# Performance work log

Hardware: AMD Instinct MI355X
Metric: run time of the kernel (lower is better)

The kernel has to match this reference:

```python
import jax, jax.numpy as jnp
import numpy as np

NEG_SLOPE = 0.1  # LeakyReLU alpha from __init__
EPS = 1e-5


def setup_inputs() -> dict:
    key = jax.random.key(0)
    k1, k2, k3, k4, k5 = jax.random.split(key, 5)
    N, E, DIN, DOUT = 10000, 160000, 1024, 1024
    x = jax.random.normal(k1, (N, DIN), dtype=jnp.float32)
    W = jax.random.normal(k2, (DIN, DOUT), dtype=jnp.float32) * 0.02  # xavier-ish gain
    a = jax.random.normal(k3, (1, 2 * DOUT), dtype=jnp.float32) * 0.02
    src = jax.random.randint(k4, (E,), 0, N, dtype=jnp.int64)  # edge rows i
    dst = jax.random.randint(k5, (E,), 0, N, dtype=jnp.int64)  # edge cols j
    return {"x": x, "W": W, "a": a, "src": src, "dst": dst}


def reference(x, W, a, src, dst):
    N = x.shape[0]
    d = W.shape[1]
    h = x @ W                                   # [N, d]
    # a @ cat(h_src, h_dst)^T == (h @ a_l)[src] + (h @ a_r)[dst]
    a_l, a_r = a[0, :d], a[0, d:]
    al = h @ a_l                                # [N]
    ar = h @ a_r                                # [N]
    e = jnp.exp(-jax.nn.leaky_relu(al[src] + ar[dst], negative_slope=NEG_SLOPE))  # [E]
    # sparse rowsum: A @ ones  ->  segment_sum of e over rows
    rowsum = jax.ops.segment_sum(e, src, num_segments=N)          # [N]
    # sparse aggregate: A @ h  (dropout = identity in eval mode)
    h_prime = jax.ops.segment_sum(e[:, None] * h[dst], src, num_segments=N)  # [N, d]
    h_prime = h_prime / (rowsum[:, None] + EPS)
    return jax.nn.elu(h_prime)  # concat=True branch
```

## Files before the change

### kernel.cpp

```cpp
#include <hip/hip_runtime.h>
#include <hip/hip_bf16.h>
#include <stdint.h>
#include <math.h>

#define DK 1024
#define DN 1024
#define CAP 64

typedef __attribute__((ext_vector_type(8))) short bf16x8;
typedef __attribute__((ext_vector_type(4))) float f32x4;

__device__ __forceinline__ unsigned short f2bf(float f) {
  union { float f; uint32_t u; } v; v.f = f;
  uint32_t r = v.u + 0x7FFFu + ((v.u >> 16) & 1u);
  return (unsigned short)(r >> 16);
}
__device__ __forceinline__ float bf2f(unsigned short b) {
  union { uint32_t u; float f; } v; v.u = ((uint32_t)b) << 16; return v.f;
}

__device__ __forceinline__ void gload_lds16(const void* g, void* l) {
  __builtin_amdgcn_global_load_lds((const __attribute__((address_space(1))) unsigned int*)g,
                                   (__attribute__((address_space(3))) unsigned int*)l,
                                   16, 0, 0);
}

__device__ __forceinline__ void block_reduce2(float& pl, float& pr) {
#pragma unroll
  for (int off = 32; off >= 1; off >>= 1) {
    pl += __shfl_down(pl, off);
    pr += __shfl_down(pr, off);
  }
  __shared__ float sl[4], sr[4];
  int w = threadIdx.x >> 6, lane = threadIdx.x & 63;
  if (lane == 0) { sl[w] = pl; sr[w] = pr; }
  __syncthreads();
  if (threadIdx.x == 0) {
    pl = sl[0] + sl[1] + sl[2] + sl[3];
    pr = sr[0] + sr[1] + sr[2] + sr[3];
  }
}

__global__ __launch_bounds__(256) void wvec_kernel(const float* __restrict__ W,
                                                   const float* __restrict__ a,
                                                   float* __restrict__ wl,
                                                   float* __restrict__ wr,
                                                   int* __restrict__ cnt, int M) {
  int idx = blockIdx.x * 256 + threadIdx.x;
  if (idx < M) cnt[idx] = 0;
  int k = blockIdx.x;
  int tid = threadIdx.x;
  float4 wv = ((const float4*)(W + (size_t)k * DN))[tid];
  float4 l4 = ((const float4*)a)[tid];
  float4 r4 = ((const float4*)(a + DN))[tid];
  float pl = wv.x * l4.x + wv.y * l4.y + wv.z * l4.z + wv.w * l4.w;
  float pr = wv.x * r4.x + wv.y * r4.y + wv.z * r4.z + wv.w * r4.w;
  block_reduce2(pl, pr);
  if (tid == 0) { wl[k] = pl; wr[k] = pr; }
}

__global__ __launch_bounds__(256) void prep_kernel(const float* __restrict__ x,
                                                   unsigned short* __restrict__ xb,
                                                   const float* __restrict__ W,
                                                   unsigned short* __restrict__ Wt,
                                                   const float* __restrict__ wl,
                                                   const float* __restrict__ wr,
                                                   float* __restrict__ al,
                                                   float* __restrict__ ar,
                                                   int M) {
  if ((int)blockIdx.x < M) {
    int row = blockIdx.x;
    int tid = threadIdx.x;
    float4 v = ((const float4*)(x + (size_t)row * DK))[tid];
    ushort4 o;
    o.x = f2bf(v.x); o.y = f2bf(v.y); o.z = f2bf(v.z); o.w = f2bf(v.w);
    ((ushort4*)(xb + (size_t)row * DK))[tid] = o;
    float4 l4 = ((const float4*)wl)[tid];
    float4 r4 = ((const float4*)wr)[tid];
    float pl = v.x * l4.x + v.y * l4.y + v.z * l4.z + v.w * l4.w;
    float pr = v.x * r4.x + v.y * r4.y + v.z * r4.z + v.w * r4.w;
    block_reduce2(pl, pr);
    if (tid == 0) { al[row] = pl; ar[row] = pr; }
  } else {
    __shared__ float t[32][33];
    int bid = blockIdx.x - M;
    int tx = threadIdx.x & 31, ty = threadIdx.x >> 5;
    int bk = (bid & 31) * 32, bn = (bid >> 5) * 32;
#pragma unroll
    for (int rr = 0; rr < 4; ++rr) {
      int row = ty + rr * 8;
      t[row][tx] = W[(size_t)(bk + row) * DN + bn + tx];
    }
    __syncthreads();
#pragma unroll
    for (int rr = 0; rr < 4; ++rr) {
      int row = ty + rr * 8;
      Wt[(size_t)(bn + row) * DK + bk + tx] = f2bf(t[tx][row]);
    }
  }
}

__global__ __launch_bounds__(256) void gemm_kernel(const unsigned short* __restrict__ A,
                                                   const unsigned short* __restrict__ Bt,
                                                   unsigned short* __restrict__ Hb,
                                                   int M) {
  __shared__ unsigned short As[128 * 32];
  __shared__ unsigned short Bs[128 * 32];
  const int tid = threadIdx.x;
  const int w = tid >> 6, lane = tid & 63;
  const int r = lane & 15, q = lane >> 4;
  const int m0 = blockIdx.x * 128, n0 = blockIdx.y * 128;
  const int wr = (w >> 1) * 64, wc = (w & 1) * 64;

  const int c0 = w * 64 + lane;
  const int rowA0 = c0 >> 2, g0 = c0 & 3;
  const int rowA1 = rowA0 + 64;
  int gr0 = m0 + rowA0; if (gr0 >= M) gr0 = M - 1;
  int gr1 = m0 + rowA1; if (gr1 >= M) gr1 = M - 1;
  const unsigned short* gA0 = A + (size_t)gr0 * DK + g0 * 8;
  const unsigned short* gA1 = A + (size_t)gr1 * DK + g0 * 8;
  const unsigned short* gB0 = Bt + (size_t)(n0 + rowA0) * DK + g0 * 8;
  const unsigned short* gB1 = Bt + (size_t)(n0 + rowA1) * DK + g0 * 8;
  unsigned short* lA0 = As + w * 512;
  unsigned short* lA1 = As + 2048 + w * 512;
  unsigned short* lB0 = Bs + w * 512;
  unsigned short* lB1 = Bs + 2048 + w * 512;

  const f32x4 zero = {0.f, 0.f, 0.f, 0.f};
  f32x4 acc[4][4];
#pragma unroll
  for (int i = 0; i < 4; ++i)
#pragma unroll
    for (int j = 0; j < 4; ++j) acc[i][j] = zero;

  for (int k0 = 0; k0 < DK; k0 += 32) {
    gload_lds16(gA0, lA0);
    gload_lds16(gA1, lA1);
    gload_lds16(gB0, lB0);
    gload_lds16(gB1, lB1);
    gA0 += 32; gA1 += 32; gB0 += 32; gB1 += 32;
    __syncthreads();

    bf16x8 af[4], bfr[4];
#pragma unroll
    for (int i = 0; i < 4; ++i)
      af[i] = *(const bf16x8*)&As[(wr + i * 16 + r) * 32 + q * 8];
#pragma unroll
    for (int j = 0; j < 4; ++j)
      bfr[j] = *(const bf16x8*)&Bs[(wc + j * 16 + r) * 32 + q * 8];
#pragma unroll
    for (int i = 0; i < 4; ++i)
#pragma unroll
      for (int j = 0; j < 4; ++j)
        acc[i][j] = __builtin_amdgcn_mfma_f32_16x16x32_bf16(af[i], bfr[j], acc[i][j], 0, 0, 0);
    __syncthreads();
  }

#pragma unroll
  for (int i = 0; i < 4; ++i) {
#pragma unroll
    for (int reg = 0; reg < 4; ++reg) {
      int m = m0 + wr + i * 16 + q * 4 + reg;
      if (m < M) {
#pragma unroll
        for (int j = 0; j < 4; ++j) {
          int n = n0 + wc + j * 16 + r;
          Hb[(size_t)m * DN + n] = f2bf(acc[i][j][reg]);
        }
      }
    }
  }
}

__global__ __launch_bounds__(256) void edge_kernel(const int* __restrict__ src,
                                                   const int* __restrict__ dst,
                                                   const float* __restrict__ al,
                                                   const float* __restrict__ ar,
                                                   int* __restrict__ cnt,
                                                   int* __restrict__ bdst,
                                                   float* __restrict__ be, int E) {
  int i = blockIdx.x * 256 + threadIdx.x;
  if (i < E) {
    int s = src[i], d = dst[i];
    float v = al[s] + ar[d];
    float lr = v > 0.f ? v : 0.1f * v;
    float e = expf(-lr);
    int pos = atomicAdd(&cnt[s], 1);
    if (pos < CAP) {
      bdst[(s << 6) + pos] = d;
      be[(s << 6) + pos] = e;
    }
  }
}

__global__ __launch_bounds__(256) void aggregate_kernel(const int* __restrict__ cnt,
                                                        const int* __restrict__ bdst,
                                                        const float* __restrict__ be,
                                                        const unsigned short* __restrict__ Hb,
                                                        float* __restrict__ out, int M) {
  int row = blockIdx.x;
  int tid = threadIdx.x;
  int n = cnt[row]; if (n > CAP) n = CAP;
  int base = row << 6;
  size_t coff = (size_t)tid * 4;
  float a0 = 0.f, a1 = 0.f, a2 = 0.f, a3 = 0.f, rs = 0.f;
  int p = 0;
  for (; p + 8 <= n; p += 8) {
    int4 da = *(const int4*)(bdst + base + p);
    int4 db = *(const int4*)(bdst + base + p + 4);
    float4 ea = *(const float4*)(be + base + p);
    float4 eb = *(const float4*)(be + base + p + 4);
    ushort4 h0 = *(const ushort4*)&Hb[(size_t)da.x * DN + coff];
    ushort4 h1 = *(const ushort4*)&Hb[(size_t)da.y * DN + coff];
    ushort4 h2 = *(const ushort4*)&Hb[(size_t)da.z * DN + coff];
    ushort4 h3 = *(const ushort4*)&Hb[(size_t)da.w * DN + coff];
    ushort4 h4 = *(const ushort4*)&Hb[(size_t)db.x * DN + coff];
    ushort4 h5 = *(const ushort4*)&Hb[(size_t)db.y * DN + coff];
    ushort4 h6 = *(const ushort4*)&Hb[(size_t)db.z * DN + coff];
    ushort4 h7 = *(const ushort4*)&Hb[(size_t)db.w * DN + coff];
    rs += ((ea.x + ea.y) + (ea.z + ea.w)) + ((eb.x + eb.y) + (eb.z + eb.w));
    a0 += ea.x * bf2f(h0.x) + ea.y * bf2f(h1.x) + ea.z * bf2f(h2.x) + ea.w * bf2f(h3.x)
        + eb.x * bf2f(h4.x) + eb.y * bf2f(h5.x) + eb.z * bf2f(h6.x) + eb.w * bf2f(h7.x);
    a1 += ea.x * bf2f(h0.y) + ea.y * bf2f(h1.y) + ea.z * bf2f(h2.y) + ea.w * bf2f(h3.y)
        + eb.x * bf2f(h4.y) + eb.y * bf2f(h5.y) + eb.z * bf2f(h6.y) + eb.w * bf2f(h7.y);
    a2 += ea.x * bf2f(h0.z) + ea.y * bf2f(h1.z) + ea.z * bf2f(h2.z) + ea.w * bf2f(h3.z)
        + eb.x * bf2f(h4.z) + eb.y * bf2f(h5.z) + eb.z * bf2f(h6.z) + eb.w * bf2f(h7.z);
    a3 += ea.x * bf2f(h0.w) + ea.y * bf2f(h1.w) + ea.z * bf2f(h2.w) + ea.w * bf2f(h3.w)
        + eb.x * bf2f(h4.w) + eb.y * bf2f(h5.w) + eb.z * bf2f(h6.w) + eb.w * bf2f(h7.w);
  }
  for (; p + 4 <= n; p += 4) {
    int4 d4 = *(const int4*)(bdst + base + p);
    float4 e4 = *(const float4*)(be + base + p);
    ushort4 h0 = *(const ushort4*)&Hb[(size_t)d4.x * DN + coff];
    ushort4 h1 = *(const ushort4*)&Hb[(size_t)d4.y * DN + coff];
    ushort4 h2 = *(const ushort4*)&Hb[(size_t)d4.z * DN + coff];
    ushort4 h3 = *(const ushort4*)&Hb[(size_t)d4.w * DN + coff];
    rs += (e4.x + e4.y) + (e4.z + e4.w);
    a0 += e4.x * bf2f(h0.x) + e4.y * bf2f(h1.x) + e4.z * bf2f(h2.x) + e4.w * bf2f(h3.x);
    a1 += e4.x * bf2f(h0.y) + e4.y * bf2f(h1.y) + e4.z * bf2f(h2.y) + e4.w * bf2f(h3.y);
    a2 += e4.x * bf2f(h0.z) + e4.y * bf2f(h1.z) + e4.z * bf2f(h2.z) + e4.w * bf2f(h3.z);
    a3 += e4.x * bf2f(h0.w) + e4.y * bf2f(h1.w) + e4.z * bf2f(h2.w) + e4.w * bf2f(h3.w);
  }
  for (; p < n; ++p) {
    int d = bdst[base + p];
    float e = be[base + p];
    rs += e;
    ushort4 hv = *(const ushort4*)&Hb[(size_t)d * DN + coff];
    a0 += e * bf2f(hv.x);
    a1 += e * bf2f(hv.y);
    a2 += e * bf2f(hv.z);
    a3 += e * bf2f(hv.w);
  }
  float inv = 1.f / (rs + 1e-5f);
  float4 o; float v;
  v = a0 * inv; o.x = v > 0.f ? v : (expf(v) - 1.f);
  v = a1 * inv; o.y = v > 0.f ? v : (expf(v) - 1.f);
  v = a2 * inv; o.z = v > 0.f ? v : (expf(v) - 1.f);
  v = a3 * inv; o.w = v > 0.f ? v : (expf(v) - 1.f);
  ((float4*)(out + (size_t)row * DN))[tid] = o;
}

extern "C" void kernel_launch(void* const* d_in, const int* in_sizes, int n_in,
                              void* d_out, int out_size, void* d_ws, size_t ws_size,
                              hipStream_t stream) {
  const float* x = (const float*)d_in[0];
  const float* W = (const float*)d_in[1];
  const float* a = (const float*)d_in[2];
  const int* src = (const int*)d_in[3];
  const int* dst = (const int*)d_in[4];
  float* out = (float*)d_out;
  const int M = in_sizes[0] / DK;
  const int E = in_sizes[3];

  size_t off = 0;
  auto alloc = [&](size_t bytes) -> void* {
    void* p = (char*)d_ws + off;
    off += (bytes + 255) & ~(size_t)255;
    return p;
  };
  unsigned short* xb   = (unsigned short*)alloc((size_t)M * DK * 2);
  unsigned short* Wt   = (unsigned short*)alloc((size_t)DK * DN * 2);
  unsigned short* Hb   = (unsigned short*)alloc((size_t)M * DN * 2);
  float*          al   = (float*)alloc((size_t)M * 4);
  float*          ar   = (float*)alloc((size_t)M * 4);
  float*          wl   = (float*)alloc((size_t)DK * 4);
  float*          wr   = (float*)alloc((size_t)DK * 4);
  int*            cnt  = (int*)alloc((size_t)M * 4);
  int*            bdst = (int*)alloc((size_t)M * CAP * 4);
  float*          be   = (float*)alloc((size_t)M * CAP * 4);

  wvec_kernel<<<DK, 256, 0, stream>>>(W, a, wl, wr, cnt, M);
  prep_kernel<<<M + (DK / 32) * (DN / 32), 256, 0, stream>>>(x, xb, W, Wt, wl, wr, al, ar, M);
  gemm_kernel<<<dim3((M + 127) / 128, DN / 128), 256, 0, stream>>>(xb, Wt, Hb, M);
  edge_kernel<<<(E + 255) / 256, 256, 0, stream>>>(src, dst, al, ar, cnt, bdst, be, E);
  aggregate_kernel<<<M, 256, 0, stream>>>(cnt, bdst, be, Hb, out, M);
}
```

Measured before the change: 196.0 us.

## Restructure aggregate: two rows per block, 16-byte gathers, batched 16-edge loads

The aggregate kernel now handles two rows per 256-thread block. Each thread covers 8 bf16 columns through one 16-byte load instead of 4 columns through an 8-byte load. Edges are processed in masked batches of 16, with all 16 neighbor-row gathers issued before any accumulation, which raises memory-level parallelism. Outputs are written with nontemporal stores. The masked batches load row 0 for padded slots, so rows with fewer than 16 edges do wasted gather work. The larger register arrays may also lower occupancy.

```diff
diff --git a/kernel.cpp b/kernel.cpp
--- a/kernel.cpp
+++ b/kernel.cpp
@@ -9,6 +9,7 @@
 
 typedef __attribute__((ext_vector_type(8))) short bf16x8;
 typedef __attribute__((ext_vector_type(4))) float f32x4;
+typedef __attribute__((ext_vector_type(8))) unsigned short u16x8;
 
 __device__ __forceinline__ unsigned short f2bf(float f) {
   union { float f; uint32_t u; } v; v.f = f;
@@ -193,71 +194,84 @@
   }
 }
 
+__device__ __forceinline__ void agg_batch16(const int* __restrict__ bdst,
+                                            const float* __restrict__ be,
+                                            const unsigned short* __restrict__ Hc,
+                                            int base, int p, int n,
+                                            float (&acc)[8], float& rs) {
+  int d[16]; float e[16];
+#pragma unroll
+  for (int u = 0; u < 4; ++u) {
+    int4 d4 = *(const int4*)(bdst + base + p + 4 * u);
+    float4 e4 = *(const float4*)(be + base + p + 4 * u);
+    d[4 * u + 0] = d4.x; d[4 * u + 1] = d4.y; d[4 * u + 2] = d4.z; d[4 * u + 3] = d4.w;
+    e[4 * u + 0] = e4.x; e[4 * u + 1] = e4.y; e[4 * u + 2] = e4.z; e[4 * u + 3] = e4.w;
+  }
+#pragma unroll
+  for (int j = 0; j < 16; ++j) {
+    bool valid = (p + j) < n;
+    d[j] = valid ? d[j] : 0;
+    e[j] = valid ? e[j] : 0.f;
+  }
+  u16x8 hv[16];
+#pragma unroll
+  for (int j = 0; j < 16; ++j)
+    hv[j] = *(const u16x8*)(Hc + (size_t)d[j] * DN);
+#pragma unroll
+  for (int j = 0; j < 16; ++j) {
+    float ej = e[j];
+    rs += ej;
+#pragma unroll
+    for (int c = 0; c < 8; ++c)
+      acc[c] += ej * bf2f(hv[j][c]);
+  }
+}
+
 __global__ __launch_bounds__(256) void aggregate_kernel(const int* __restrict__ cnt,
                                                         const int* __restrict__ bdst,
                                                         const float* __restrict__ be,
                                                         const unsigned short* __restrict__ Hb,
                                                         float* __restrict__ out, int M) {
-  int row = blockIdx.x;
-  int tid = threadIdx.x;
+  int row = (blockIdx.x << 1) + (threadIdx.x >> 7);
+  if (row >= M) return;
+  int t = threadIdx.x & 127;
   int n = cnt[row]; if (n > CAP) n = CAP;
   int base = row << 6;
-  size_t coff = (size_t)tid * 4;
-  float a0 = 0.f, a1 = 0.f, a2 = 0.f, a3 = 0.f, rs = 0.f;
-  int p = 0;
-  for (; p + 8 <= n; p += 8) {
-    int4 da = *(const int4*)(bdst + base + p);
-    int4 db = *(const int4*)(bdst + base + p + 4);
-    float4 ea = *(const float4*)(be + base + p);
-    float4 eb = *(const float4*)(be + base + p + 4);
-    ushort4 h0 = *(const ushort4*)&Hb[(size_t)da.x * DN + coff];
-    ushort4 h1 = *(const ushort4*)&Hb[(size_t)da.y * DN + coff];
-    ushort4 h2 = *(const ushort4*)&Hb[(size_t)da.z * DN + coff];
-    ushort4 h3 = *(const ushort4*)&Hb[(size_t)da.w * DN + coff];
-    ushort4 h4 = *(const ushort4*)&Hb[(size_t)db.x * DN + coff];
-    ushort4 h5 = *(const ushort4*)&Hb[(size_t)db.y * DN + coff];
-    ushort4 h6 = *(const ushort4*)&Hb[(size_t)db.z * DN + coff];
-    ushort4 h7 = *(const ushort4*)&Hb[(size_t)db.w * DN + coff];
-    rs += ((ea.x + ea.y) + (ea.z + ea.w)) + ((eb.x + eb.y) + (eb.z + eb.w));
-    a0 += ea.x * bf2f(h0.x) + ea.y * bf2f(h1.x) + ea.z * bf2f(h2.x) + ea.w * bf2f(h3.x)
-        + eb.x * bf2f(h4.x) + eb.y * bf2f(h5.x) + eb.z * bf2f(h6.x) + eb.w * bf2f(h7.x);
-    a1 += ea.x * bf2f(h0.y) + ea.y * bf2f(h1.y) + ea.z * bf2f(h2.y) + ea.w * bf2f(h3.y)
-        + eb.x * bf2f(h4.y) + eb.y * bf2f(h5.y) + eb.z * bf2f(h6.y) + eb.w * bf2f(h7.y);
-    a2 += ea.x * bf2f(h0.z) + ea.y * bf2f(h1.z) + ea.z * bf2f(h2.z) + ea.w * bf2f(h3.z)
-        + eb.x * bf2f(h4.z) + eb.y * bf2f(h5.z) + eb.z * bf2f(h6.z) + eb.w * bf2f(h7.z);
-    a3 += ea.x * bf2f(h0.w) + ea.y * bf2f(h1.w) + ea.z * bf2f(h2.w) + ea.w * bf2f(h3.w)
-        + eb.x * bf2f(h4.w) + eb.y * bf2f(h5.w) + eb.z * bf2f(h6.w) + eb.w * bf2f(h7.w);
-  }
-  for (; p + 4 <= n; p += 4) {
-    int4 d4 = *(const int4*)(bdst + base + p);
-    float4 e4 = *(const float4*)(be + base + p);
-    ushort4 h0 = *(const ushort4*)&Hb[(size_t)d4.x * DN + coff];
-    ushort4 h1 = *(const ushort4*)&Hb[(size_t)d4.y * DN + coff];
-    ushort4 h2 = *(const ushort4*)&Hb[(size_t)d4.z * DN + coff];
-    ushort4 h3 = *(const ushort4*)&Hb[(size_t)d4.w * DN + coff];
-    rs += (e4.x + e4.y) + (e4.z + e4.w);
-    a0 += e4.x * bf2f(h0.x) + e4.y * bf2f(h1.x) + e4.z * bf2f(h2.x) + e4.w * bf2f(h3.x);
-    a1 += e4.x * bf2f(h0.y) + e4.y * bf2f(h1.y) + e4.z * bf2f(h2.y) + e4.w * bf2f(h3.y);
-    a2 += e4.x * bf2f(h0.z) + e4.y * bf2f(h1.z) + e4.z * bf2f(h2.z) + e4.w * bf2f(h3.z);
-    a3 += e4.x * bf2f(h0.w) + e4.y * bf2f(h1.w) + e4.z * bf2f(h2.w) + e4.w * bf2f(h3.w);
-  }
-  for (; p < n; ++p) {
-    int d = bdst[base + p];
-    float e = be[base + p];
-    rs += e;
-    ushort4 hv = *(const ushort4*)&Hb[(size_t)d * DN + coff];
-    a0 += e * bf2f(hv.x);
-    a1 += e * bf2f(hv.y);
-    a2 += e * bf2f(hv.z);
-    a3 += e * bf2f(hv.w);
-  }
+  size_t coff = (size_t)t * 8;
+  const unsigned short* Hc = Hb + coff;
+  float acc[8] = {0.f, 0.f, 0.f, 0.f, 0.f, 0.f, 0.f, 0.f};
+  float rs = 0.f;
+
+  agg_batch16(bdst, be, Hc, base, 0, n, acc, rs);
+  if (n > 16)
+    agg_batch16(bdst, be, Hc, base, 16, n, acc, rs);
+  if (n > 32) {
+    for (int p = 32; p < n; ++p) {
+      int dd = bdst[base + p];
+      float ee = be[base + p];
+      rs += ee;
+      u16x8 hvv = *(const u16x8*)(Hc + (size_t)dd * DN);
+#pragma unroll
+      for (int c = 0; c < 8; ++c)
+        acc[c] += ee * bf2f(hvv[c]);
+    }
+  }
+
   float inv = 1.f / (rs + 1e-5f);
-  float4 o; float v;
-  v = a0 * inv; o.x = v > 0.f ? v : (expf(v) - 1.f);
-  v = a1 * inv; o.y = v > 0.f ? v : (expf(v) - 1.f);
-  v = a2 * inv; o.z = v > 0.f ? v : (expf(v) - 1.f);
-  v = a3 * inv; o.w = v > 0.f ? v : (expf(v) - 1.f);
-  ((float4*)(out + (size_t)row * DN))[tid] = o;
+  f32x4 lo, hi;
+#pragma unroll
+  for (int c = 0; c < 4; ++c) {
+    float v = acc[c] * inv;
+    lo[c] = v > 0.f ? v : (expf(v) - 1.f);
+  }
+#pragma unroll
+  for (int c = 0; c < 4; ++c) {
+    float v = acc[c + 4] * inv;
+    hi[c] = v > 0.f ? v : (expf(v) - 1.f);
+  }
+  f32x4* op = (f32x4*)(out + (size_t)row * DN + coff);
+  __builtin_nontemporal_store(lo, op);
+  __builtin_nontemporal_store(hi, op + 1);
 }
 
 extern "C" void kernel_launch(void* const* d_in, const int* in_sizes, int n_in,
@@ -293,5 +307,5 @@
   prep_kernel<<<M + (DK / 32) * (DN / 32), 256, 0, stream>>>(x, xb, W, Wt, wl, wr, al, ar, M);
   gemm_kernel<<<dim3((M + 127) / 128, DN / 128), 256, 0, stream>>>(xb, Wt, Hb, M);
   edge_kernel<<<(E + 255) / 256, 256, 0, stream>>>(src, dst, al, ar, cnt, bdst, be, E);
-  aggregate_kernel<<<M, 256, 0, stream>>>(cnt, bdst, be, Hb, out, M);
-}
+  aggregate_kernel<<<(M + 1) / 2, 256, 0, stream>>>(cnt, bdst, be, Hb, out, M);
+}
```

After: 194.0 us. About the same (-1.0%).
